# Optimization experiments

Measured on AMD Instinct MI355X. Metric: run time of the kernel, lower is better.

Reference implementation:

```python
import jax, jax.numpy as jnp
import numpy as np
import math

B, H, LQ, LK, D = 2, 16, 2048, 2048, 128

def setup_inputs() -> dict:
    key = jax.random.key(0)
    kq, kk, kv, km = jax.random.split(key, 4)
    return {
        "query": jax.random.normal(kq, (B, H, LQ, D), dtype=jnp.float32),
        "key": jax.random.normal(kk, (B, H, LK, D), dtype=jnp.float32),
        "value": jax.random.normal(kv, (B, H, LK, D), dtype=jnp.float32),
        # positive integer multiplicities in [1, 8] so log() is finite
        "key_multiplicities": jax.random.randint(km, (B, LK), 1, 9, dtype=jnp.int32),
    }

def reference(query, key, value, key_multiplicities):
    scale = 1.0 / math.sqrt(query.shape[-1])
    # scores: [B, H, Lq, Lk]
    scores = jnp.einsum("bhqd,bhkd->bhqk", query, key) * scale
    # additive log-multiplicity bias, broadcast over heads and queries
    log_mult = jnp.log(key_multiplicities.astype(scores.dtype))  # [B, Lk]
    scores = scores + log_mult[:, None, None, :]
    attn = jax.nn.softmax(scores, axis=-1)
    # dropout_p = 0.0 -> identity
    return jnp.einsum("bhqk,bhkd->bhqd", attn, value)
```

## Files before the change

### kernel.cpp

```cpp
#include <hip/hip_runtime.h>
#include <hip/hip_bf16.h>

constexpr int B_  = 2;
constexpr int H_  = 16;
constexpr int LQ_ = 2048;
constexpr int LK_ = 2048;
constexpr int D_  = 128;

constexpr int BM = 128;
constexpr int BN = 64;

constexpr float SCALE_LOG2E = 0.12751649734586414f;

typedef short s16x4 __attribute__((ext_vector_type(4)));
typedef short s16x8 __attribute__((ext_vector_type(8)));
typedef float f32x4 __attribute__((ext_vector_type(4)));

#define MFMA16 __builtin_amdgcn_mfma_f32_16x16x32_bf16

#if __has_builtin(__builtin_amdgcn_exp2f)
#define EXP2(x) __builtin_amdgcn_exp2f(x)
#else
#define EXP2(x) exp2f(x)
#endif
#if __has_builtin(__builtin_amdgcn_logf)
#define LOG2(x) __builtin_amdgcn_logf(x)
#else
#define LOG2(x) log2f(x)
#endif

static __device__ __forceinline__ int pk2bf(float a, float b) {
  float2 t{a, b};
  __hip_bfloat162 h = __float22bfloat162_rn(t);
  return *reinterpret_cast<int*>(&h);
}

__global__ __launch_bounds__(256, 2)
void attn_fwd(const float* __restrict__ qg, const float* __restrict__ kg,
              const float* __restrict__ vg, const int* __restrict__ multg,
              float* __restrict__ outg) {
  __shared__ alignas(16) short Ksh[64 * 128];
  __shared__ alignas(16) short Vsh[128 * 64];
  __shared__ alignas(16) short Psh[128 * 64];
  __shared__ alignas(16) float biasSh[LK_];
  __shared__ alignas(16) float xferSh[4][2][16];

  const int tid  = threadIdx.x;
  const int w    = tid >> 6;
  const int lane = tid & 63;
  const int c    = lane & 15;
  const int qd   = lane >> 4;

  const int L   = blockIdx.y * gridDim.x + blockIdx.x;
  const int k8  = L >> 3;
  const int qb  = k8 & 15;
  const int bh  = (L & 7) * 4 + (k8 >> 4);
  const int b   = bh >> 4;

  const float* qptr = qg + (size_t)bh * LQ_ * D_;
  const float* kptr = kg + (size_t)bh * LK_ * D_;
  const float* vptr = vg + (size_t)bh * LK_ * D_;
  float*       optr = outg + (size_t)bh * LQ_ * D_;
  const int*   mptr = multg + b * LK_;

  for (int i = tid; i < LK_; i += 256)
    biasSh[i] = LOG2((float)mptr[i]);

  const int q0 = qb * BM + w * 32;
  s16x8 qf[2][4];
#pragma unroll
  for (int qs = 0; qs < 2; ++qs) {
    const float* qrow = qptr + (size_t)(q0 + qs * 16 + c) * D_ + qd * 8;
#pragma unroll
    for (int kf = 0; kf < 4; ++kf) {
      float4 a  = *(const float4*)(qrow + kf * 32);
      float4 bq = *(const float4*)(qrow + kf * 32 + 4);
      int4 t;
      t.x = pk2bf(a.x * SCALE_LOG2E, a.y * SCALE_LOG2E);
      t.y = pk2bf(a.z * SCALE_LOG2E, a.w * SCALE_LOG2E);
      t.z = pk2bf(bq.x * SCALE_LOG2E, bq.y * SCALE_LOG2E);
      t.w = pk2bf(bq.z * SCALE_LOG2E, bq.w * SCALE_LOG2E);
      qf[qs][kf] = *(s16x8*)&t;
    }
  }

  f32x4 o[2][8];
  float m_r[2], l_r[2];
#pragma unroll
  for (int qs = 0; qs < 2; ++qs) {
#pragma unroll
    for (int dt = 0; dt < 8; ++dt) o[qs][dt] = (f32x4){0.f, 0.f, 0.f, 0.f};
    m_r[qs] = -INFINITY; l_r[qs] = 0.f;
  }

  for (int kt = 0; kt < LK_ / BN; ++kt) {
    const int k0 = kt * BN;
    __syncthreads();

#pragma unroll
    for (int i = 0; i < 8; ++i) {
      int f4  = tid + i * 256;
      int row = f4 >> 5;
      int d0  = (f4 & 31) * 4;
      float4 a = *(const float4*)(kptr + (size_t)(k0 + row) * D_ + d0);
      int2 pk;
      pk.x = pk2bf(a.x, a.y);
      pk.y = pk2bf(a.z, a.w);
      int pos = (d0 >> 3) ^ (row & 15);
      *(int2*)&Ksh[row * 128 + pos * 8 + (d0 & 4)] = pk;
    }

#pragma unroll
    for (int r = 0; r < 2; ++r) {
      int kgrp = w + r * 4;
      float2 f2v[8];
      const float* vrow = vptr + (size_t)(k0 + kgrp * 8) * D_ + 2 * lane;
#pragma unroll
      for (int j = 0; j < 8; ++j)
        f2v[j] = *(const float2*)(vrow + (size_t)j * D_);
#pragma unroll
      for (int half = 0; half < 2; ++half) {
        int4 t;
        t.x = pk2bf(half ? f2v[0].y : f2v[0].x, half ? f2v[1].y : f2v[1].x);
        t.y = pk2bf(half ? f2v[2].y : f2v[2].x, half ? f2v[3].y : f2v[3].x);
        t.z = pk2bf(half ? f2v[4].y : f2v[4].x, half ? f2v[5].y : f2v[5].x);
        t.w = pk2bf(half ? f2v[6].y : f2v[6].x, half ? f2v[7].y : f2v[7].x);
        int d   = 2 * lane + half;
        int pos = kgrp ^ (lane & 7);
        *(int4*)&Vsh[d * 64 + pos * 8] = t;
      }
    }
    __syncthreads();

    f32x4 St[2][4];
#pragma unroll
    for (int qs = 0; qs < 2; ++qs)
#pragma unroll
      for (int ct = 0; ct < 4; ++ct) St[qs][ct] = (f32x4){0.f, 0.f, 0.f, 0.f};

#pragma unroll
    for (int ct = 0; ct < 4; ++ct) {
      const short* kb = &Ksh[(ct * 16 + c) * 128];
#pragma unroll
      for (int kf = 0; kf < 4; ++kf) {
        s16x8 kfr = *(const s16x8*)&kb[((kf * 4 + qd) ^ c) * 8];
        St[0][ct] = MFMA16(kfr, qf[0][kf], St[0][ct], 0, 0, 0);
        St[1][ct] = MFMA16(kfr, qf[1][kf], St[1][ct], 0, 0, 0);
      }
    }

    float bvf[4][4];
#pragma unroll
    for (int ct = 0; ct < 4; ++ct) {
      float4 bv = *(const float4*)&biasSh[k0 + ct * 16 + qd * 4];
      bvf[ct][0] = bv.x; bvf[ct][1] = bv.y; bvf[ct][2] = bv.z; bvf[ct][3] = bv.w;
    }

#pragma unroll
    for (int qs = 0; qs < 2; ++qs) {
      float x[4][4];
#pragma unroll
      for (int ct = 0; ct < 4; ++ct)
#pragma unroll
        for (int reg = 0; reg < 4; ++reg)
          x[ct][reg] = St[qs][ct][reg] + bvf[ct][reg];

      float mx = x[0][0];
#pragma unroll
      for (int ct = 0; ct < 4; ++ct)
#pragma unroll
        for (int reg = 0; reg < 4; ++reg) mx = fmaxf(mx, x[ct][reg]);
      mx = fmaxf(mx, __shfl_xor(mx, 16));
      mx = fmaxf(mx, __shfl_xor(mx, 32));

      float mn    = fmaxf(m_r[qs], mx);
      float alpha = EXP2(m_r[qs] - mn);
      m_r[qs] = mn;

      float rs = 0.f;
#pragma unroll
      for (int ct = 0; ct < 4; ++ct)
#pragma unroll
        for (int reg = 0; reg < 4; ++reg) {
          float p = EXP2(x[ct][reg] - mn);
          x[ct][reg] = p;
          rs += p;
        }
      rs += __shfl_xor(rs, 16);
      rs += __shfl_xor(rs, 32);
      l_r[qs] = l_r[qs] * alpha + rs;

      const int pr = w * 32 + qs * 16 + c;
#pragma unroll
      for (int ct = 0; ct < 4; ++ct) {
        int2 pk;
        pk.x = pk2bf(x[ct][0], x[ct][1]);
        pk.y = pk2bf(x[ct][2], x[ct][3]);
        int pos = (ct * 2 + (qd >> 1)) ^ (pr & 7);
        *(int2*)&Psh[pr * 64 + pos * 8 + (qd & 1) * 4] = pk;
      }

      if (qd == 0) xferSh[w][qs][c] = alpha;
    }

#pragma unroll
    for (int qs = 0; qs < 2; ++qs) {
      float4 a4 = *(const float4*)&xferSh[w][qs][qd * 4];
      float ar[4] = {a4.x, a4.y, a4.z, a4.w};
#pragma unroll
      for (int dt = 0; dt < 8; ++dt)
#pragma unroll
        for (int reg = 0; reg < 4; ++reg) o[qs][dt][reg] *= ar[reg];
    }

    s16x8 pf[2][2];
#pragma unroll
    for (int qs = 0; qs < 2; ++qs) {
      const int pr = w * 32 + qs * 16 + c;
#pragma unroll
      for (int kf = 0; kf < 2; ++kf) {
        int pos = (kf * 4 + qd) ^ (pr & 7);
        pf[qs][kf] = *(const s16x8*)&Psh[pr * 64 + pos * 8];
      }
    }
#pragma unroll
    for (int dt = 0; dt < 8; ++dt) {
      int d = dt * 16 + c;
      const short* vb = &Vsh[d * 64];
      s16x8 vf[2];
#pragma unroll
      for (int kf = 0; kf < 2; ++kf)
        vf[kf] = *(const s16x8*)&vb[((kf * 4 + qd) ^ ((d >> 1) & 7)) * 8];
#pragma unroll
      for (int qs = 0; qs < 2; ++qs)
#pragma unroll
        for (int kf = 0; kf < 2; ++kf)
          o[qs][dt] = MFMA16(pf[qs][kf], vf[kf], o[qs][dt], 0, 0, 0);
    }
  }

  if (qd == 0) { xferSh[w][0][c] = l_r[0]; xferSh[w][1][c] = l_r[1]; }
#pragma unroll
  for (int qs = 0; qs < 2; ++qs) {
    float4 l4 = *(const float4*)&xferSh[w][qs][qd * 4];
    float lr[4] = {l4.x, l4.y, l4.z, l4.w};
#pragma unroll
    for (int reg = 0; reg < 4; ++reg) {
      float inv = 1.0f / lr[reg];
      int row = q0 + qs * 16 + qd * 4 + reg;
      float* orow = optr + (size_t)row * D_ + c;
#pragma unroll
      for (int dt = 0; dt < 8; ++dt) orow[dt * 16] = o[qs][dt][reg] * inv;
    }
  }
}

extern "C" void kernel_launch(void* const* d_in, const int* in_sizes, int n_in,
                              void* d_out, int out_size, void* d_ws, size_t ws_size,
                              hipStream_t stream) {
  const float* q = (const float*)d_in[0];
  const float* k = (const float*)d_in[1];
  const float* v = (const float*)d_in[2];
  const int* mult = (const int*)d_in[3];
  float* out = (float*)d_out;

  dim3 grid(LQ_ / BM, B_ * H_);
  dim3 block(256);
  attn_fwd<<<grid, block, 0, stream>>>(q, k, v, mult, out);
}
```

Measured before the change: 244.4 us.

## Pre-convert K/V to swizzled bf16 and double-buffer tiles via async LDS DMA

New measurement: 231.5 us. -5.3%, faster.

```diff
diff --git a/kernel.cpp b/kernel.cpp
--- a/kernel.cpp
+++ b/kernel.cpp
@@ -9,6 +9,8 @@
 
 constexpr int BM = 128;
 constexpr int BN = 64;
+constexpr int NT = LK_ / BN;
+constexpr int TILE_SH = 64 * 128;
 
 constexpr float SCALE_LOG2E = 0.12751649734586414f;
 
@@ -35,15 +37,77 @@
   return *reinterpret_cast<int*>(&h);
 }
 
+static __device__ __forceinline__ void dma16(const short* g, short* l) {
+  __builtin_amdgcn_global_load_lds(
+      (const __attribute__((address_space(1))) void*)g,
+      (__attribute__((address_space(3))) void*)l, 16, 0, 0);
+}
+
+__global__ __launch_bounds__(256)
+void prep(const float* __restrict__ kg, const float* __restrict__ vg,
+          const int* __restrict__ multg, short* __restrict__ wsK,
+          short* __restrict__ wsV, float* __restrict__ wsBias) {
+  __shared__ float tileF[64 * 133];
+  const int tid = threadIdx.x;
+  const int wg  = blockIdx.x;
+  const float* kp = kg + (size_t)wg * 64 * 128;
+  const float* vp = vg + (size_t)wg * 64 * 128;
+  short* wk = wsK + (size_t)wg * TILE_SH;
+  short* wv = wsV + (size_t)wg * TILE_SH;
+
+#pragma unroll
+  for (int i = 0; i < 4; ++i) {
+    int idx = tid + i * 256;
+    int row = idx >> 4, blk = idx & 15;
+    const float* src = kp + row * 128 + blk * 8;
+    float4 a = *(const float4*)src;
+    float4 c4 = *(const float4*)(src + 4);
+    int4 t;
+    t.x = pk2bf(a.x, a.y);  t.y = pk2bf(a.z, a.w);
+    t.z = pk2bf(c4.x, c4.y); t.w = pk2bf(c4.z, c4.w);
+    int pos = blk ^ (row & 15);
+    *(int4*)&wk[row * 128 + pos * 8] = t;
+  }
+
+#pragma unroll
+  for (int i = 0; i < 8; ++i) {
+    int idx = tid + i * 256;
+    int key = idx >> 5, d0 = (idx & 31) * 4;
+    float4 a = *(const float4*)(vp + key * 128 + d0);
+    float* dst = &tileF[key * 133 + d0];
+    dst[0] = a.x; dst[1] = a.y; dst[2] = a.z; dst[3] = a.w;
+  }
+  __syncthreads();
+#pragma unroll
+  for (int i = 0; i < 4; ++i) {
+    int idx = tid + i * 256;
+    int d = idx >> 3, kgrp = idx & 7;
+    float v[8];
+#pragma unroll
+    for (int j = 0; j < 8; ++j) v[j] = tileF[(kgrp * 8 + j) * 133 + d];
+    int4 t;
+    t.x = pk2bf(v[0], v[1]); t.y = pk2bf(v[2], v[3]);
+    t.z = pk2bf(v[4], v[5]); t.w = pk2bf(v[6], v[7]);
+    int pos = kgrp ^ ((d >> 1) & 7);
+    *(int4*)&wv[d * 64 + pos * 8] = t;
+  }
+
+  if (wg < 8) {
+    int b = wg >> 2;
+    for (int j = tid; j < 512; j += 256) {
+      int i0 = (wg & 3) * 512 + j;
+      wsBias[b * LK_ + i0] = LOG2((float)multg[b * LK_ + i0]);
+    }
+  }
+}
+
 __global__ __launch_bounds__(256, 2)
-void attn_fwd(const float* __restrict__ qg, const float* __restrict__ kg,
-              const float* __restrict__ vg, const int* __restrict__ multg,
+void attn_fwd(const float* __restrict__ qg, const short* __restrict__ wsK,
+              const short* __restrict__ wsV, const float* __restrict__ wsBias,
               float* __restrict__ outg) {
-  __shared__ alignas(16) short Ksh[64 * 128];
-  __shared__ alignas(16) short Vsh[128 * 64];
+  __shared__ alignas(16) short Kbuf[2][TILE_SH];
+  __shared__ alignas(16) short Vbuf[2][TILE_SH];
   __shared__ alignas(16) short Psh[128 * 64];
-  __shared__ alignas(16) float biasSh[LK_];
-  __shared__ alignas(16) float xferSh[4][2][16];
 
   const int tid  = threadIdx.x;
   const int w    = tid >> 6;
@@ -58,13 +122,10 @@
   const int b   = bh >> 4;
 
   const float* qptr = qg + (size_t)bh * LQ_ * D_;
-  const float* kptr = kg + (size_t)bh * LK_ * D_;
-  const float* vptr = vg + (size_t)bh * LK_ * D_;
   float*       optr = outg + (size_t)bh * LQ_ * D_;
-  const int*   mptr = multg + b * LK_;
-
-  for (int i = tid; i < LK_; i += 256)
-    biasSh[i] = LOG2((float)mptr[i]);
+  const short* kws  = wsK + (size_t)bh * NT * TILE_SH;
+  const short* vws  = wsV + (size_t)bh * NT * TILE_SH;
+  const float* bias = wsBias + b * LK_;
 
   const int q0 = qb * BM + w * 32;
   s16x8 qf[2][4];
@@ -93,44 +154,30 @@
     m_r[qs] = -INFINITY; l_r[qs] = 0.f;
   }
 
-  for (int kt = 0; kt < LK_ / BN; ++kt) {
-    const int k0 = kt * BN;
-    __syncthreads();
-
-#pragma unroll
-    for (int i = 0; i < 8; ++i) {
-      int f4  = tid + i * 256;
-      int row = f4 >> 5;
-      int d0  = (f4 & 31) * 4;
-      float4 a = *(const float4*)(kptr + (size_t)(k0 + row) * D_ + d0);
-      int2 pk;
-      pk.x = pk2bf(a.x, a.y);
-      pk.y = pk2bf(a.z, a.w);
-      int pos = (d0 >> 3) ^ (row & 15);
-      *(int2*)&Ksh[row * 128 + pos * 8 + (d0 & 4)] = pk;
-    }
-
-#pragma unroll
-    for (int r = 0; r < 2; ++r) {
-      int kgrp = w + r * 4;
-      float2 f2v[8];
-      const float* vrow = vptr + (size_t)(k0 + kgrp * 8) * D_ + 2 * lane;
-#pragma unroll
-      for (int j = 0; j < 8; ++j)
-        f2v[j] = *(const float2*)(vrow + (size_t)j * D_);
-#pragma unroll
-      for (int half = 0; half < 2; ++half) {
-        int4 t;
-        t.x = pk2bf(half ? f2v[0].y : f2v[0].x, half ? f2v[1].y : f2v[1].x);
-        t.y = pk2bf(half ? f2v[2].y : f2v[2].x, half ? f2v[3].y : f2v[3].x);
-        t.z = pk2bf(half ? f2v[4].y : f2v[4].x, half ? f2v[5].y : f2v[5].x);
-        t.w = pk2bf(half ? f2v[6].y : f2v[6].x, half ? f2v[7].y : f2v[7].x);
-        int d   = 2 * lane + half;
-        int pos = kgrp ^ (lane & 7);
-        *(int4*)&Vsh[d * 64 + pos * 8] = t;
-      }
-    }
-    __syncthreads();
+  auto dmaKV = [&](int kt, int bb) {
+    const short* gK = kws + (size_t)kt * TILE_SH;
+    const short* gV = vws + (size_t)kt * TILE_SH;
+#pragma unroll
+    for (int i = 0; i < 4; ++i) {
+      int off = (w * 4 + i) * 512;
+      dma16(gK + off + lane * 8, &Kbuf[bb][off]);
+      dma16(gV + off + lane * 8, &Vbuf[bb][off]);
+    }
+  };
+
+  dmaKV(0, 0);
+  __syncthreads();
+
+  for (int kt = 0; kt < NT; ++kt) {
+    const int cur = kt & 1;
+    if (kt + 1 < NT) dmaKV(kt + 1, cur ^ 1);
+
+    float bvf[4][4];
+#pragma unroll
+    for (int ct = 0; ct < 4; ++ct) {
+      float4 bv = *(const float4*)&bias[kt * BN + ct * 16 + qd * 4];
+      bvf[ct][0] = bv.x; bvf[ct][1] = bv.y; bvf[ct][2] = bv.z; bvf[ct][3] = bv.w;
+    }
 
     f32x4 St[2][4];
 #pragma unroll
@@ -140,20 +187,13 @@
 
 #pragma unroll
     for (int ct = 0; ct < 4; ++ct) {
-      const short* kb = &Ksh[(ct * 16 + c) * 128];
+      const short* kb = &Kbuf[cur][(ct * 16 + c) * 128];
 #pragma unroll
       for (int kf = 0; kf < 4; ++kf) {
         s16x8 kfr = *(const s16x8*)&kb[((kf * 4 + qd) ^ c) * 8];
         St[0][ct] = MFMA16(kfr, qf[0][kf], St[0][ct], 0, 0, 0);
         St[1][ct] = MFMA16(kfr, qf[1][kf], St[1][ct], 0, 0, 0);
       }
-    }
-
-    float bvf[4][4];
-#pragma unroll
-    for (int ct = 0; ct < 4; ++ct) {
-      float4 bv = *(const float4*)&biasSh[k0 + ct * 16 + qd * 4];
-      bvf[ct][0] = bv.x; bvf[ct][1] = bv.y; bvf[ct][2] = bv.z; bvf[ct][3] = bv.w;
     }
 
 #pragma unroll
@@ -200,13 +240,9 @@
         *(int2*)&Psh[pr * 64 + pos * 8 + (qd & 1) * 4] = pk;
       }
 
-      if (qd == 0) xferSh[w][qs][c] = alpha;
-    }
-
-#pragma unroll
-    for (int qs = 0; qs < 2; ++qs) {
-      float4 a4 = *(const float4*)&xferSh[w][qs][qd * 4];
-      float ar[4] = {a4.x, a4.y, a4.z, a4.w};
+      float ar[4];
+#pragma unroll
+      for (int reg = 0; reg < 4; ++reg) ar[reg] = __shfl(alpha, qd * 4 + reg);
 #pragma unroll
       for (int dt = 0; dt < 8; ++dt)
 #pragma unroll
@@ -226,7 +262,7 @@
 #pragma unroll
     for (int dt = 0; dt < 8; ++dt) {
       int d = dt * 16 + c;
-      const short* vb = &Vsh[d * 64];
+      const short* vb = &Vbuf[cur][d * 64];
       s16x8 vf[2];
 #pragma unroll
       for (int kf = 0; kf < 2; ++kf)
@@ -237,13 +273,15 @@
         for (int kf = 0; kf < 2; ++kf)
           o[qs][dt] = MFMA16(pf[qs][kf], vf[kf], o[qs][dt], 0, 0, 0);
     }
-  }
-
-  if (qd == 0) { xferSh[w][0][c] = l_r[0]; xferSh[w][1][c] = l_r[1]; }
+
+    __syncthreads();
+  }
+
 #pragma unroll
   for (int qs = 0; qs < 2; ++qs) {
-    float4 l4 = *(const float4*)&xferSh[w][qs][qd * 4];
-    float lr[4] = {l4.x, l4.y, l4.z, l4.w};
+    float lr[4];
+#pragma unroll
+    for (int reg = 0; reg < 4; ++reg) lr[reg] = __shfl(l_r[qs], qd * 4 + reg);
 #pragma unroll
     for (int reg = 0; reg < 4; ++reg) {
       float inv = 1.0f / lr[reg];
@@ -264,7 +302,13 @@
   const int* mult = (const int*)d_in[3];
   float* out = (float*)d_out;
 
+  constexpr size_t KV_BYTES = (size_t)B_ * H_ * LK_ * D_ * 2;
+  short* wsK = (short*)d_ws;
+  short* wsV = (short*)((char*)d_ws + KV_BYTES);
+  float* wsBias = (float*)((char*)d_ws + 2 * KV_BYTES);
+
+  prep<<<dim3(B_ * H_ * NT), dim3(256), 0, stream>>>(k, v, mult, wsK, wsV, wsBias);
+
   dim3 grid(LQ_ / BM, B_ * H_);
-  dim3 block(256);
-  attn_fwd<<<grid, block, 0, stream>>>(q, k, v, mult, out);
-}
+  attn_fwd<<<grid, dim3(256), 0, stream>>>(q, wsK, wsV, wsBias, out);
+}
```
